# Performance work log

Hardware: AMD Instinct MI355X
Metric: run time of the kernel (lower is better)

## Reference

```python
import jax, jax.numpy as jnp
import numpy as np

N = 100000   # nodes
E = 1600000  # edges (avg degree 16)
IN, HID, OUT = 128, 128, 64
EPS = 1e-5


def setup_inputs() -> dict:
    key = jax.random.key(0)
    ks = jax.random.split(key, 16)
    x = jax.random.normal(ks[0], (N, IN), jnp.float32)
    edge_index = jax.random.randint(ks[1], (2, E), 0, N, dtype=jnp.int64)
    edge_weight = jax.random.uniform(ks[2], (E,), jnp.float32)

    def lin(k, o, i):
        return jax.random.normal(k, (o, i), jnp.float32) / np.float32(np.sqrt(i))

    return {
        "x": x, "edge_index": edge_index, "edge_weight": edge_weight,
        # SGConv linear layers
        "W1": lin(ks[3], HID, IN), "b1": jnp.zeros((HID,), jnp.float32),
        "W2": lin(ks[4], HID, HID), "b2": jnp.zeros((HID,), jnp.float32),
        "W3": lin(ks[5], OUT, HID), "b3": jnp.zeros((OUT,), jnp.float32),
        # BatchNorm affine params (nontrivial values for a meaningful reference)
        "g1": 1.0 + 0.1 * jax.random.normal(ks[6], (HID,), jnp.float32),
        "be1": 0.1 * jax.random.normal(ks[7], (HID,), jnp.float32),
        "g2": 1.0 + 0.1 * jax.random.normal(ks[8], (HID,), jnp.float32),
        "be2": 0.1 * jax.random.normal(ks[9], (HID,), jnp.float32),
        # proj MLP
        "pW1": lin(ks[10], HID, HID), "pb1": jnp.zeros((HID,), jnp.float32),
        "pW2": lin(ks[11], HID, HID), "pb2": jnp.zeros((HID,), jnp.float32),
    }


def reference(x, edge_index, edge_weight, W1, b1, W2, b2, W3, b3,
              g1, be1, g2, be2, pW1, pb1, pW2, pb2):
    src, dst = edge_index[0], edge_index[1]

    def propagate(h):
        # SGConv K=1, normalize=False: edge-weighted scatter-sum over neighbors
        msg = h[src] * edge_weight[:, None]          # [E, d]
        return jax.ops.segment_sum(msg, dst, num_segments=N)

    def bn(h, g, b):
        # BatchNorm1d, training-mode batch statistics (biased variance)
        m = h.mean(axis=0)
        v = h.var(axis=0)
        return (h - m) * jax.lax.rsqrt(v + EPS) * g + b

    h = x
    h = propagate(h) @ W1.T + b1
    h = jax.nn.relu(bn(h, g1, be1))                  # dropout = identity (eval)
    h = propagate(h) @ W2.T + b2
    h = jax.nn.relu(bn(h, g2, be2))

    # proj: Linear -> Dropout(identity) -> ReLU -> Linear
    z = jax.nn.relu(h @ pW1.T + pb1) @ pW2.T + pb2
    logits = propagate(h) @ W3.T + b3
    return (logits, h, z)
```

## Files before the change

### kernel.cpp

```cpp
#include <hip/hip_runtime.h>


#define NF 128
#define BCAP 6144

using short8   = __attribute__((ext_vector_type(8))) short;
using ushort8v = __attribute__((ext_vector_type(8))) unsigned short;
using f32x4    = __attribute__((ext_vector_type(4))) float;

__device__ __forceinline__ float b2f(unsigned short u) {
    return __uint_as_float(((unsigned)u) << 16);
}
__device__ __forceinline__ unsigned short f2b(float f) {
    unsigned u = __float_as_uint(f);
    u += 0x7fff + ((u >> 16) & 1);
    return (unsigned short)(u >> 16);
}


__global__ __launch_bounds__(512) void filla2_k(const int* __restrict__ ei,
                                                const float* __restrict__ ew,
                                                int* __restrict__ bcur,
                                                int2* __restrict__ tmp, int E)
{
    __shared__ int dstg[4096];
    __shared__ int cnt[512];
    __shared__ int base[512];
    int t = threadIdx.x;
    cnt[t] = 0;
    __syncthreads();
    int e0 = blockIdx.x * 4096;
    int eend = min(e0 + 4096, E);
    int n = eend - e0;
    for (int i = t; i < n; i += 512) {
        int d = ei[E + e0 + i];
        dstg[i] = d;
        atomicAdd(&cnt[d >> 8], 1);
    }
    __syncthreads();
    {
        int c = cnt[t];
        base[t] = c ? (t * BCAP + atomicAdd(&bcur[t], c)) : 0;
        cnt[t] = 0;
    }
    __syncthreads();
    for (int i = t; i < n; i += 512) {
        int d = dstg[i];
        int b = d >> 8;
        int r = atomicAdd(&cnt[b], 1);
        int2 q;
        q.x = (int)(((unsigned)ei[e0 + i]) | (((unsigned)(d & 255)) << 24));
        q.y = __float_as_int(ew[e0 + i]);
        tmp[base[b] + r] = q;
    }
}

__global__ __launch_bounds__(512) void bscan_k(const int* __restrict__ bcnt,
                                               int* __restrict__ bbase, int nbuk)
{
    __shared__ int sc[512];
    int t = threadIdx.x;
    int v = (t < nbuk) ? bcnt[t] : 0;
    sc[t] = v;
    __syncthreads();
    for (int ofs = 1; ofs < 512; ofs <<= 1) {
        int x = (t >= ofs) ? sc[t - ofs] : 0;
        __syncthreads();
        sc[t] += x;
        __syncthreads();
    }
    if (t < nbuk) bbase[t] = sc[t] - v;
}

__global__ __launch_bounds__(512) void fillb_k(const int2* __restrict__ tmp,
                                               const int* __restrict__ bbase,
                                               const int* __restrict__ bcnt,
                                               int* __restrict__ off,
                                               int2* __restrict__ epk,
                                               int N, int E, int nbuk)
{
    __shared__ int lcnt[256];
    __shared__ int lcur[256];
    int t = threadIdx.x;
    int b = blockIdx.x;
    int lo = b << 8;
    int nn = min(256, N - lo);
    if (t < 256) lcnt[t] = 0;
    __syncthreads();
    const int2* src = tmp + (size_t)b * BCAP;
    int cntb = bcnt[b];
    int s = bbase[b];
    for (int i = t; i < cntb; i += 512)
        atomicAdd(&lcnt[((unsigned)src[i].x) >> 24], 1);
    __syncthreads();
    int v = (t < 256) ? lcnt[t] : 0;
    for (int ofs = 1; ofs < 256; ofs <<= 1) {
        int x = (t >= ofs && t < 256) ? lcnt[t - ofs] : 0;
        __syncthreads();
        if (t < 256) lcnt[t] += x;
        __syncthreads();
    }
    if (t < 256) {
        int st = s + lcnt[t] - v;
        lcur[t] = st;
        if (t < nn) off[lo + t] = st;
    }
    if (b == 0 && t == 0) off[N] = E;
    __syncthreads();
    for (int i = t; i < cntb; i += 512) {
        int2 q = src[i];
        unsigned qx = (unsigned)q.x;
        int pos = atomicAdd(&lcur[qx >> 24], 1);
        int2 o;
        o.x = (int)(qx & 0xFFFFFF);
        o.y = q.y;
        epk[pos] = o;
    }
}

__global__ __launch_bounds__(256) void convx_k(const float* __restrict__ x,
                                               unsigned short* __restrict__ xb,
                                               int total4)
{
    int idx = blockIdx.x * 256 + threadIdx.x;
    if (idx >= total4) return;
    float4 v = *(const float4*)&x[(size_t)idx * 4];
    ushort4 o;
    o.x = f2b(v.x); o.y = f2b(v.y); o.z = f2b(v.z); o.w = f2b(v.w);
    *(ushort4*)&xb[(size_t)idx * 4] = o;
}

__global__ __launch_bounds__(64) void convw_all_k(
    const float* __restrict__ W1,  const float* __restrict__ W2,
    const float* __restrict__ pW1, const float* __restrict__ pW2,
    const float* __restrict__ W3,
    unsigned short* __restrict__ W1b,  unsigned short* __restrict__ W2b,
    unsigned short* __restrict__ pW1b, unsigned short* __restrict__ pW2b,
    unsigned short* __restrict__ W3b)
{
    int bid = blockIdx.x;
    const float* W; unsigned short* Wb; int lb;
    if      (bid < 32)  { W = W1;  Wb = W1b;  lb = bid; }
    else if (bid < 64)  { W = W2;  Wb = W2b;  lb = bid - 32; }
    else if (bid < 96)  { W = pW1; Wb = pW1b; lb = bid - 64; }
    else if (bid < 128) { W = pW2; Wb = pW2b; lb = bid - 96; }
    else                { W = W3;  Wb = W3b;  lb = bid - 128; }
    int lane = threadIdx.x;
    int nb = lb >> 2, ks = lb & 3;
    const float* src = W + (size_t)(nb * 16 + (lane & 15)) * 128 + ks * 32 + (lane >> 4) * 8;
    unsigned short* dst = Wb + ((size_t)lb * 64 + lane) * 8;
#pragma unroll
    for (int j = 0; j < 8; j++) dst[j] = f2b(src[j]);
}

template <int BN>
__global__ __launch_bounds__(256) void gather_k(
    const unsigned short* __restrict__ h, const int* __restrict__ off,
    const int2* __restrict__ epk, unsigned short* __restrict__ p, int N,
    const float* __restrict__ bnstats, const float* __restrict__ g,
    const float* __restrict__ be, float invN)
{
    int row = blockIdx.x * 4 + (threadIdx.x >> 6);
    if (row >= N) return;
    int lane = threadIdx.x & 63;
    int half = lane >> 4;
    int sub  = lane & 15;
    int c0 = sub * 8;

    float sc[8], sh[8];
#pragma unroll
    for (int j = 0; j < 8; j++) { sc[j] = 1.f; sh[j] = 0.f; }
    if (BN) {
#pragma unroll
        for (int j = 0; j < 8; j++) {
            float m = bnstats[c0 + j] * invN;
            float v = bnstats[NF + c0 + j] * invN - m * m;
            float r = rsqrtf(v + 1e-5f) * g[c0 + j];
            sc[j] = r; sh[j] = be[c0 + j] - m * r;
        }
    }

    int beg = off[row], end = off[row + 1];
    float a[8];
#pragma unroll
    for (int j = 0; j < 8; j++) a[j] = 0.f;

#define PROC_EDGE(qq, uu)                                                     \
    {                                                                         \
        float w = __int_as_float((qq).y);                                     \
        _Pragma("unroll")                                                     \
        for (int j = 0; j < 8; j++) {                                         \
            float v = b2f((unsigned short)(uu)[j]);                           \
            if (BN) v = fmaxf(fmaf(v, sc[j], sh[j]), 0.f);                    \
            a[j] = fmaf(v, w, a[j]);                                          \
        }                                                                     \
    }

    int e = beg;
    for (; e + 16 <= end; e += 16) {
        int2 q0 = epk[e + 0 + half],  q1 = epk[e + 4 + half];
        int2 q2 = epk[e + 8 + half],  q3 = epk[e + 12 + half];
        ushort8v u0 = *(const ushort8v*)&h[(size_t)q0.x * NF + c0];
        ushort8v u1 = *(const ushort8v*)&h[(size_t)q1.x * NF + c0];
        ushort8v u2 = *(const ushort8v*)&h[(size_t)q2.x * NF + c0];
        ushort8v u3 = *(const ushort8v*)&h[(size_t)q3.x * NF + c0];
        PROC_EDGE(q0, u0); PROC_EDGE(q1, u1);
        PROC_EDGE(q2, u2); PROC_EDGE(q3, u3);
    }
    for (; e + 4 <= end; e += 4) {
        int2 q = epk[e + half];
        ushort8v u = *(const ushort8v*)&h[(size_t)q.x * NF + c0];
        PROC_EDGE(q, u);
    }
    if (half < end - e) {
        int2 q = epk[e + half];
        ushort8v u = *(const ushort8v*)&h[(size_t)q.x * NF + c0];
        PROC_EDGE(q, u);
    }
#undef PROC_EDGE

#pragma unroll
    for (int j = 0; j < 8; j++) {
        a[j] += __shfl_xor(a[j], 16);
        a[j] += __shfl_xor(a[j], 32);
    }

    if (half == 0) {
        ushort8v o;
#pragma unroll
        for (int j = 0; j < 8; j++) o[j] = f2b(a[j]);
        *(ushort8v*)&p[(size_t)row * NF + c0] = o;
    }
}

__global__ __launch_bounds__(256) void gather64_k(
    const unsigned short* __restrict__ y, const int* __restrict__ off,
    const int2* __restrict__ epk, const float* __restrict__ bias,
    float* __restrict__ out, int N)
{
    int row = blockIdx.x * 4 + (threadIdx.x >> 6);
    if (row >= N) return;
    int lane = threadIdx.x & 63;
    int str = lane >> 4;
    int sub = lane & 15;
    int c0 = sub * 4;

    int beg = off[row], end = off[row + 1];
    float a[4] = {0.f, 0.f, 0.f, 0.f};

#define PROC_E64(qq, uu)                                                      \
    {                                                                         \
        float w = __int_as_float((qq).y);                                     \
        a[0] = fmaf(b2f((uu).x), w, a[0]);                                    \
        a[1] = fmaf(b2f((uu).y), w, a[1]);                                    \
        a[2] = fmaf(b2f((uu).z), w, a[2]);                                    \
        a[3] = fmaf(b2f((uu).w), w, a[3]);                                    \
    }

    int e = beg;
    for (; e + 16 <= end; e += 16) {
        int2 q0 = epk[e + 0 + str],  q1 = epk[e + 4 + str];
        int2 q2 = epk[e + 8 + str],  q3 = epk[e + 12 + str];
        ushort4 u0 = *(const ushort4*)&y[(size_t)q0.x * 64 + c0];
        ushort4 u1 = *(const ushort4*)&y[(size_t)q1.x * 64 + c0];
        ushort4 u2 = *(const ushort4*)&y[(size_t)q2.x * 64 + c0];
        ushort4 u3 = *(const ushort4*)&y[(size_t)q3.x * 64 + c0];
        PROC_E64(q0, u0); PROC_E64(q1, u1);
        PROC_E64(q2, u2); PROC_E64(q3, u3);
    }
    for (; e + 4 <= end; e += 4) {
        int2 q = epk[e + str];
        ushort4 u = *(const ushort4*)&y[(size_t)q.x * 64 + c0];
        PROC_E64(q, u);
    }
    if (str < end - e) {
        int2 q = epk[e + str];
        ushort4 u = *(const ushort4*)&y[(size_t)q.x * 64 + c0];
        PROC_E64(q, u);
    }
#undef PROC_E64

#pragma unroll
    for (int j = 0; j < 4; j++) {
        a[j] += __shfl_xor(a[j], 16);
        a[j] += __shfl_xor(a[j], 32);
    }

    if (lane < 16) {
        float4 o;
        o.x = a[0] + bias[c0];     o.y = a[1] + bias[c0 + 1];
        o.z = a[2] + bias[c0 + 2]; o.w = a[3] + bias[c0 + 3];
        *(float4*)&out[(size_t)row * 64 + c0] = o;
    }
}

template <int M, int COUT>
__global__ __launch_bounds__(256) void mgemm_k(
    const unsigned short* __restrict__ A, const unsigned short* __restrict__ Wb,
    const float* __restrict__ bias, void* __restrict__ Cp,
    int N, int relu, float* __restrict__ stats)
{
    constexpr int MI = (M == 128) ? 4 : 2;
    __shared__ float sbuf[256];

    const int tid = threadIdx.x, wid = tid >> 6, lane = tid & 63;
    const int quad = lane >> 4, l16 = lane & 15;
    const int rowBase = blockIdx.x * 128;
    int r0, c0;
    if constexpr (M == 128) { r0 = (wid >> 1) * 64; c0 = (wid & 1) * 64; }
    else                    { r0 = wid * 32;        c0 = 0; }

    f32x4 acc[MI][4];
#pragma unroll
    for (int mi = 0; mi < MI; mi++)
#pragma unroll
        for (int ni = 0; ni < 4; ni++)
#pragma unroll
            for (int r = 0; r < 4; r++) acc[mi][ni][r] = 0.f;

#pragma unroll
    for (int ks = 0; ks < 4; ++ks) {
        short8 af[MI], bf[4];
#pragma unroll
        for (int mi = 0; mi < MI; mi++) {
            int gr = rowBase + r0 + mi * 16 + l16;
            gr = (gr < N) ? gr : (N - 1);
            af[mi] = *(const short8*)(A + (size_t)gr * 128 + ks * 32 + quad * 8);
        }
#pragma unroll
        for (int ni = 0; ni < 4; ni++) {
            int nb = (c0 >> 4) + ni;
            bf[ni] = *(const short8*)(Wb + ((size_t)(nb * 4 + ks) * 64 + lane) * 8);
        }
#pragma unroll
        for (int mi = 0; mi < MI; mi++)
#pragma unroll
            for (int ni = 0; ni < 4; ni++)
                acc[mi][ni] = __builtin_amdgcn_mfma_f32_16x16x32_bf16(
                    af[mi], bf[ni], acc[mi][ni], 0, 0, 0);
    }

    float csum[4] = {0.f, 0.f, 0.f, 0.f}, csq[4] = {0.f, 0.f, 0.f, 0.f};
#pragma unroll
    for (int mi = 0; mi < MI; mi++) {
#pragma unroll
        for (int r = 0; r < 4; r++) {
            int gr = rowBase + r0 + mi * 16 + quad * 4 + r;
            if (gr >= N) continue;
#pragma unroll
            for (int ni = 0; ni < 4; ni++) {
                int col = c0 + ni * 16 + l16;
                float v = acc[mi][ni][r] + (bias ? bias[col] : 0.f);
                if (relu) v = fmaxf(v, 0.f);
                if constexpr (COUT == 1)
                    ((unsigned short*)Cp)[(size_t)gr * M + col] = f2b(v);
                else
                    ((float*)Cp)[(size_t)gr * M + col] = v;
                csum[ni] += v;
                csq[ni]  += v * v;
            }
        }
    }

    if (stats) {
        sbuf[tid] = 0.f;
        __syncthreads();
#pragma unroll
        for (int ni = 0; ni < 4; ni++) {
            int col = c0 + ni * 16 + l16;
            atomicAdd(&sbuf[col], csum[ni]);
            atomicAdd(&sbuf[128 + col], csq[ni]);
        }
        __syncthreads();
        if (tid < 128) {
            unsafeAtomicAdd(&stats[tid], sbuf[tid]);
            unsafeAtomicAdd(&stats[NF + tid], sbuf[128 + tid]);
        }
    }
}

__global__ __launch_bounds__(256) void bnrelu2_k(
    const unsigned short* __restrict__ pre, const float* __restrict__ stats,
    const float* __restrict__ g, const float* __restrict__ be,
    float* __restrict__ outh, unsigned short* __restrict__ hb,
    int total4, float invN)
{
    int idx = blockIdx.x * 256 + threadIdx.x;
    if (idx >= total4) return;
    int c = (idx * 4) & 127;
    ushort4 u = *(const ushort4*)&pre[(size_t)idx * 4];
    float in[4] = {b2f(u.x), b2f(u.y), b2f(u.z), b2f(u.w)};
    float o[4];
#pragma unroll
    for (int i = 0; i < 4; i++) {
        float m   = stats[c + i] * invN;
        float var = stats[NF + c + i] * invN - m * m;
        float rs  = rsqrtf(var + 1e-5f);
        o[i] = fmaxf((in[i] - m) * rs * g[c + i] + be[c + i], 0.f);
    }
    float4 f; f.x = o[0]; f.y = o[1]; f.z = o[2]; f.w = o[3];
    *(float4*)&outh[(size_t)idx * 4] = f;
    ushort4 h4;
    h4.x = f2b(o[0]); h4.y = f2b(o[1]); h4.z = f2b(o[2]); h4.w = f2b(o[3]);
    *(ushort4*)&hb[(size_t)idx * 4] = h4;
}

__global__ __launch_bounds__(256) void projf_k(
    const unsigned short* __restrict__ A, const unsigned short* __restrict__ W1b,
    const float* __restrict__ bias1, const unsigned short* __restrict__ W2b,
    const float* __restrict__ bias2, float* __restrict__ Z, int N)
{
    __shared__ unsigned short tbuf[128][136];

    const int tid = threadIdx.x, wid = tid >> 6, lane = tid & 63;
    const int quad = lane >> 4, l16 = lane & 15;
    const int rowBase = blockIdx.x * 128;
    const int r0 = (wid >> 1) * 64, c0 = (wid & 1) * 64;

    f32x4 acc[4][4];
#pragma unroll
    for (int mi = 0; mi < 4; mi++)
#pragma unroll
        for (int ni = 0; ni < 4; ni++)
#pragma unroll
            for (int r = 0; r < 4; r++) acc[mi][ni][r] = 0.f;

#pragma unroll
    for (int ks = 0; ks < 4; ++ks) {
        short8 af[4], bf[4];
#pragma unroll
        for (int mi = 0; mi < 4; mi++) {
            int gr = rowBase + r0 + mi * 16 + l16;
            gr = (gr < N) ? gr : (N - 1);
            af[mi] = *(const short8*)(A + (size_t)gr * 128 + ks * 32 + quad * 8);
        }
#pragma unroll
        for (int ni = 0; ni < 4; ni++) {
            int nb = (c0 >> 4) + ni;
            bf[ni] = *(const short8*)(W1b + ((size_t)(nb * 4 + ks) * 64 + lane) * 8);
        }
#pragma unroll
        for (int mi = 0; mi < 4; mi++)
#pragma unroll
            for (int ni = 0; ni < 4; ni++)
                acc[mi][ni] = __builtin_amdgcn_mfma_f32_16x16x32_bf16(
                    af[mi], bf[ni], acc[mi][ni], 0, 0, 0);
    }
#pragma unroll
    for (int mi = 0; mi < 4; mi++)
#pragma unroll
        for (int r = 0; r < 4; r++) {
            int lr = r0 + mi * 16 + quad * 4 + r;
#pragma unroll
            for (int ni = 0; ni < 4; ni++) {
                int col = c0 + ni * 16 + l16;
                float v = fmaxf(acc[mi][ni][r] + bias1[col], 0.f);
                tbuf[lr][col] = f2b(v);
            }
        }
    __syncthreads();

#pragma unroll
    for (int mi = 0; mi < 4; mi++)
#pragma unroll
        for (int ni = 0; ni < 4; ni++)
#pragma unroll
            for (int r = 0; r < 4; r++) acc[mi][ni][r] = 0.f;

#pragma unroll
    for (int ks = 0; ks < 4; ++ks) {
        short8 af[4], bf[4];
#pragma unroll
        for (int mi = 0; mi < 4; mi++)
            af[mi] = *(const short8*)&tbuf[r0 + mi * 16 + l16][ks * 32 + quad * 8];
#pragma unroll
        for (int ni = 0; ni < 4; ni++) {
            int nb = (c0 >> 4) + ni;
            bf[ni] = *(const short8*)(W2b + ((size_t)(nb * 4 + ks) * 64 + lane) * 8);
        }
#pragma unroll
        for (int mi = 0; mi < 4; mi++)
#pragma unroll
            for (int ni = 0; ni < 4; ni++)
                acc[mi][ni] = __builtin_amdgcn_mfma_f32_16x16x32_bf16(
                    af[mi], bf[ni], acc[mi][ni], 0, 0, 0);
    }
#pragma unroll
    for (int mi = 0; mi < 4; mi++)
#pragma unroll
        for (int r = 0; r < 4; r++) {
            int gr = rowBase + r0 + mi * 16 + quad * 4 + r;
            if (gr >= N) continue;
#pragma unroll
            for (int ni = 0; ni < 4; ni++) {
                int col = c0 + ni * 16 + l16;
                Z[(size_t)gr * 128 + col] = acc[mi][ni][r] + bias2[col];
            }
        }
}

extern "C" void kernel_launch(void* const* d_in, const int* in_sizes, int n_in,
                              void* d_out, int out_size, void* d_ws, size_t ws_size,
                              hipStream_t stream)
{
    const float* x   = (const float*)d_in[0];
    const int*   ei  = (const int*)d_in[1];
    const float* ew  = (const float*)d_in[2];
    const float* W1  = (const float*)d_in[3];
    const float* b1  = (const float*)d_in[4];
    const float* W2  = (const float*)d_in[5];
    const float* b2  = (const float*)d_in[6];
    const float* W3  = (const float*)d_in[7];
    const float* b3  = (const float*)d_in[8];
    const float* g1  = (const float*)d_in[9];
    const float* be1 = (const float*)d_in[10];
    const float* g2  = (const float*)d_in[11];
    const float* be2 = (const float*)d_in[12];
    const float* pW1 = (const float*)d_in[13];
    const float* pb1 = (const float*)d_in[14];
    const float* pW2 = (const float*)d_in[15];
    const float* pb2 = (const float*)d_in[16];

    const int N = in_sizes[0] / NF;
    const int E = in_sizes[2];

    float* out_logits = (float*)d_out;
    float* out_h      = out_logits + (size_t)N * 64;
    float* out_z      = out_h + (size_t)N * NF;

    const size_t rowsUS = (size_t)N * NF;
    int2*           epk = (int2*)d_ws;
    unsigned short* B1  = (unsigned short*)(epk + E);
    unsigned short* B2  = B1 + rowsUS;
    unsigned short* B3  = B2 + rowsUS;
    float* stats1 = (float*)(B3 + rowsUS);
    float* stats2 = stats1 + 256;
    int*   bcur   = (int*)(stats2 + 256);
    int*   bbase  = bcur + 512;
    unsigned short* W1b  = (unsigned short*)(bbase + 512);
    unsigned short* W2b  = W1b + 128 * 128;
    unsigned short* pW1b = W2b + 128 * 128;
    unsigned short* pW2b = pW1b + 128 * 128;
    unsigned short* W3b  = pW2b + 128 * 128;
    int* off = (int*)(W3b + 64 * 128);
    int2* tmp = (int2*)B2;

    const int nbuk   = (N + 255) >> 8;
    const int ggrid  = (N + 127) / 128;
    const int pgrid  = (N + 3) / 4;
    const int c4grid = (N * NF / 4 + 255) / 256;
    const int e4grid = (E + 4095) / 4096;
    const float invN = 1.f / (float)N;

    hipMemsetAsync(stats1, 0, (2 * 256) * sizeof(float) + 512 * sizeof(int), stream);

    convx_k<<<c4grid, 256, 0, stream>>>(x, B1, N * NF / 4);
    convw_all_k<<<176, 64, 0, stream>>>(W1, W2, pW1, pW2, W3,
                                        W1b, W2b, pW1b, pW2b, W3b);

    filla2_k<<<e4grid, 512, 0, stream>>>(ei, ew, bcur, tmp, E);
    bscan_k<<<1, 512, 0, stream>>>(bcur, bbase, nbuk);
    fillb_k<<<nbuk, 512, 0, stream>>>(tmp, bbase, bcur, off, epk, N, E, nbuk);

    gather_k<0><<<pgrid, 256, 0, stream>>>(B1, off, epk, B2, N,
                                           nullptr, nullptr, nullptr, 0.f);
    mgemm_k<128, 1><<<ggrid, 256, 0, stream>>>(B2, W1b, b1, B3, N, 0, stats1);

    gather_k<1><<<pgrid, 256, 0, stream>>>(B3, off, epk, B2, N,
                                           stats1, g1, be1, invN);
    mgemm_k<128, 1><<<ggrid, 256, 0, stream>>>(B2, W2b, b2, B1, N, 0, stats2);

    bnrelu2_k<<<c4grid, 256, 0, stream>>>(B1, stats2, g2, be2, out_h, B2,
                                          N * NF / 4, invN);

    mgemm_k<64, 1><<<ggrid, 256, 0, stream>>>(B2, W3b, nullptr, B3, N, 0, nullptr);
    gather64_k<<<pgrid, 256, 0, stream>>>(B3, off, epk, b3, out_logits, N);

    projf_k<<<ggrid, 256, 0, stream>>>(B2, pW1b, pb1, pW2b, pb2, out_z, N);
}
```

Baseline: 589.3 us.

## Fuse W3 projection into proj MLP kernel and pack bf16 unpack with vector FMAs

The W3 GEMM (h @ W3^T) is folded into the proj-MLP kernel, so the h tile is read by one kernel instead of two and one launch goes away. The gather kernels now load neighbor rows as packed 32-bit words, unpack bf16 pairs with a shift and a mask, and accumulate with two-wide float FMAs, which may let the compiler emit packed FMA instructions. The fused kernel writes Y with scalar per-element stores rather than vectorized ones, and carries more register pressure from holding the extra accumulators.

```diff
diff --git a/kernel.cpp b/kernel.cpp
--- a/kernel.cpp
+++ b/kernel.cpp
@@ -6,7 +6,10 @@
 
 using short8   = __attribute__((ext_vector_type(8))) short;
 using ushort8v = __attribute__((ext_vector_type(8))) unsigned short;
+using uint4v   = __attribute__((ext_vector_type(4))) unsigned int;
+using uint2v   = __attribute__((ext_vector_type(2))) unsigned int;
 using f32x4    = __attribute__((ext_vector_type(4))) float;
+using f32x2    = __attribute__((ext_vector_type(2))) float;
 
 __device__ __forceinline__ float b2f(unsigned short u) {
     return __uint_as_float(((unsigned)u) << 16);
@@ -16,7 +19,6 @@
     u += 0x7fff + ((u >> 16) & 1);
     return (unsigned short)(u >> 16);
 }
-
 
 __global__ __launch_bounds__(512) void filla2_k(const int* __restrict__ ei,
                                                 const float* __restrict__ ew,
@@ -167,32 +169,39 @@
     int sub  = lane & 15;
     int c0 = sub * 8;
 
-    float sc[8], sh[8];
-#pragma unroll
-    for (int j = 0; j < 8; j++) { sc[j] = 1.f; sh[j] = 0.f; }
+    f32x2 sc2[4], sh2[4];
     if (BN) {
 #pragma unroll
         for (int j = 0; j < 8; j++) {
             float m = bnstats[c0 + j] * invN;
             float v = bnstats[NF + c0 + j] * invN - m * m;
             float r = rsqrtf(v + 1e-5f) * g[c0 + j];
-            sc[j] = r; sh[j] = be[c0 + j] - m * r;
+            sc2[j >> 1][j & 1] = r;
+            sh2[j >> 1][j & 1] = be[c0 + j] - m * r;
         }
     }
 
     int beg = off[row], end = off[row + 1];
-    float a[8];
-#pragma unroll
-    for (int j = 0; j < 8; j++) a[j] = 0.f;
+    f32x2 acc2[4];
+#pragma unroll
+    for (int j = 0; j < 4; j++) { acc2[j][0] = 0.f; acc2[j][1] = 0.f; }
 
 #define PROC_EDGE(qq, uu)                                                     \
     {                                                                         \
         float w = __int_as_float((qq).y);                                     \
+        f32x2 w2; w2[0] = w; w2[1] = w;                                       \
         _Pragma("unroll")                                                     \
-        for (int j = 0; j < 8; j++) {                                         \
-            float v = b2f((unsigned short)(uu)[j]);                           \
-            if (BN) v = fmaxf(fmaf(v, sc[j], sh[j]), 0.f);                    \
-            a[j] = fmaf(v, w, a[j]);                                          \
+        for (int j = 0; j < 4; j++) {                                         \
+            unsigned d = (uu)[j];                                             \
+            f32x2 v;                                                          \
+            v[0] = __uint_as_float(d << 16);                                  \
+            v[1] = __uint_as_float(d & 0xffff0000u);                          \
+            if (BN) {                                                         \
+                v = __builtin_elementwise_fma(v, sc2[j], sh2[j]);             \
+                v[0] = fmaxf(v[0], 0.f);                                      \
+                v[1] = fmaxf(v[1], 0.f);                                      \
+            }                                                                 \
+            acc2[j] = __builtin_elementwise_fma(v, w2, acc2[j]);              \
         }                                                                     \
     }
 
@@ -200,25 +209,28 @@
     for (; e + 16 <= end; e += 16) {
         int2 q0 = epk[e + 0 + half],  q1 = epk[e + 4 + half];
         int2 q2 = epk[e + 8 + half],  q3 = epk[e + 12 + half];
-        ushort8v u0 = *(const ushort8v*)&h[(size_t)q0.x * NF + c0];
-        ushort8v u1 = *(const ushort8v*)&h[(size_t)q1.x * NF + c0];
-        ushort8v u2 = *(const ushort8v*)&h[(size_t)q2.x * NF + c0];
-        ushort8v u3 = *(const ushort8v*)&h[(size_t)q3.x * NF + c0];
+        uint4v u0 = *(const uint4v*)&h[(size_t)q0.x * NF + c0];
+        uint4v u1 = *(const uint4v*)&h[(size_t)q1.x * NF + c0];
+        uint4v u2 = *(const uint4v*)&h[(size_t)q2.x * NF + c0];
+        uint4v u3 = *(const uint4v*)&h[(size_t)q3.x * NF + c0];
         PROC_EDGE(q0, u0); PROC_EDGE(q1, u1);
         PROC_EDGE(q2, u2); PROC_EDGE(q3, u3);
     }
     for (; e + 4 <= end; e += 4) {
         int2 q = epk[e + half];
-        ushort8v u = *(const ushort8v*)&h[(size_t)q.x * NF + c0];
+        uint4v u = *(const uint4v*)&h[(size_t)q.x * NF + c0];
         PROC_EDGE(q, u);
     }
     if (half < end - e) {
         int2 q = epk[e + half];
-        ushort8v u = *(const ushort8v*)&h[(size_t)q.x * NF + c0];
+        uint4v u = *(const uint4v*)&h[(size_t)q.x * NF + c0];
         PROC_EDGE(q, u);
     }
 #undef PROC_EDGE
 
+    float a[8];
+#pragma unroll
+    for (int j = 0; j < 4; j++) { a[2 * j] = acc2[j][0]; a[2 * j + 1] = acc2[j][1]; }
 #pragma unroll
     for (int j = 0; j < 8; j++) {
         a[j] += __shfl_xor(a[j], 16);
@@ -246,40 +258,47 @@
     int c0 = sub * 4;
 
     int beg = off[row], end = off[row + 1];
-    float a[4] = {0.f, 0.f, 0.f, 0.f};
+    f32x2 acc2[2];
+    acc2[0][0] = 0.f; acc2[0][1] = 0.f; acc2[1][0] = 0.f; acc2[1][1] = 0.f;
 
 #define PROC_E64(qq, uu)                                                      \
     {                                                                         \
         float w = __int_as_float((qq).y);                                     \
-        a[0] = fmaf(b2f((uu).x), w, a[0]);                                    \
-        a[1] = fmaf(b2f((uu).y), w, a[1]);                                    \
-        a[2] = fmaf(b2f((uu).z), w, a[2]);                                    \
-        a[3] = fmaf(b2f((uu).w), w, a[3]);                                    \
+        f32x2 w2; w2[0] = w; w2[1] = w;                                       \
+        _Pragma("unroll")                                                     \
+        for (int j = 0; j < 2; j++) {                                         \
+            unsigned d = (uu)[j];                                             \
+            f32x2 v;                                                          \
+            v[0] = __uint_as_float(d << 16);                                  \
+            v[1] = __uint_as_float(d & 0xffff0000u);                          \
+            acc2[j] = __builtin_elementwise_fma(v, w2, acc2[j]);              \
+        }                                                                     \
     }
 
     int e = beg;
     for (; e + 16 <= end; e += 16) {
         int2 q0 = epk[e + 0 + str],  q1 = epk[e + 4 + str];
         int2 q2 = epk[e + 8 + str],  q3 = epk[e + 12 + str];
-        ushort4 u0 = *(const ushort4*)&y[(size_t)q0.x * 64 + c0];
-        ushort4 u1 = *(const ushort4*)&y[(size_t)q1.x * 64 + c0];
-        ushort4 u2 = *(const ushort4*)&y[(size_t)q2.x * 64 + c0];
-        ushort4 u3 = *(const ushort4*)&y[(size_t)q3.x * 64 + c0];
+        uint2v u0 = *(const uint2v*)&y[(size_t)q0.x * 64 + c0];
+        uint2v u1 = *(const uint2v*)&y[(size_t)q1.x * 64 + c0];
+        uint2v u2 = *(const uint2v*)&y[(size_t)q2.x * 64 + c0];
+        uint2v u3 = *(const uint2v*)&y[(size_t)q3.x * 64 + c0];
         PROC_E64(q0, u0); PROC_E64(q1, u1);
         PROC_E64(q2, u2); PROC_E64(q3, u3);
     }
     for (; e + 4 <= end; e += 4) {
         int2 q = epk[e + str];
-        ushort4 u = *(const ushort4*)&y[(size_t)q.x * 64 + c0];
+        uint2v u = *(const uint2v*)&y[(size_t)q.x * 64 + c0];
         PROC_E64(q, u);
     }
     if (str < end - e) {
         int2 q = epk[e + str];
-        ushort4 u = *(const ushort4*)&y[(size_t)q.x * 64 + c0];
+        uint2v u = *(const uint2v*)&y[(size_t)q.x * 64 + c0];
         PROC_E64(q, u);
     }
 #undef PROC_E64
 
+    float a[4] = {acc2[0][0], acc2[0][1], acc2[1][0], acc2[1][1]};
 #pragma unroll
     for (int j = 0; j < 4; j++) {
         a[j] += __shfl_xor(a[j], 16);
@@ -405,16 +424,62 @@
     *(ushort4*)&hb[(size_t)idx * 4] = h4;
 }
 
-__global__ __launch_bounds__(256) void projf_k(
+__global__ __launch_bounds__(256) void projf3_k(
     const unsigned short* __restrict__ A, const unsigned short* __restrict__ W1b,
     const float* __restrict__ bias1, const unsigned short* __restrict__ W2b,
-    const float* __restrict__ bias2, float* __restrict__ Z, int N)
+    const float* __restrict__ bias2, const unsigned short* __restrict__ W3b,
+    float* __restrict__ Z, unsigned short* __restrict__ Y, int N)
 {
     __shared__ unsigned short tbuf[128][136];
 
     const int tid = threadIdx.x, wid = tid >> 6, lane = tid & 63;
     const int quad = lane >> 4, l16 = lane & 15;
     const int rowBase = blockIdx.x * 128;
+
+    {
+        const int r0y = wid * 32;
+        f32x4 acy[2][4];
+#pragma unroll
+        for (int mi = 0; mi < 2; mi++)
+#pragma unroll
+            for (int ni = 0; ni < 4; ni++)
+#pragma unroll
+                for (int r = 0; r < 4; r++) acy[mi][ni][r] = 0.f;
+
+#pragma unroll
+        for (int ks = 0; ks < 4; ++ks) {
+            short8 af[2], bf[4];
+#pragma unroll
+            for (int mi = 0; mi < 2; mi++) {
+                int gr = rowBase + r0y + mi * 16 + l16;
+                gr = (gr < N) ? gr : (N - 1);
+                af[mi] = *(const short8*)(A + (size_t)gr * 128 + ks * 32 + quad * 8);
+            }
+#pragma unroll
+            for (int ni = 0; ni < 4; ni++)
+                bf[ni] = *(const short8*)(W3b + ((size_t)(ni * 4 + ks) * 64 + lane) * 8);
+#pragma unroll
+            for (int mi = 0; mi < 2; mi++)
+#pragma unroll
+                for (int ni = 0; ni < 4; ni++)
+                    acy[mi][ni] = __builtin_amdgcn_mfma_f32_16x16x32_bf16(
+                        af[mi], bf[ni], acy[mi][ni], 0, 0, 0);
+        }
+
+#pragma unroll
+        for (int mi = 0; mi < 2; mi++)
+#pragma unroll
+            for (int r = 0; r < 4; r++) {
+                int gr = rowBase + r0y + mi * 16 + quad * 4 + r;
+                if (gr >= N) continue;
+#pragma unroll
+                for (int ni = 0; ni < 4; ni++) {
+                    int col = ni * 16 + l16;
+                    Y[(size_t)gr * 64 + col] = f2b(acy[mi][ni][r] + 0.f);
+                }
+            }
+    }
+
     const int r0 = (wid >> 1) * 64, c0 = (wid & 1) * 64;
 
     f32x4 acc[4][4];
@@ -573,8 +638,8 @@
     bnrelu2_k<<<c4grid, 256, 0, stream>>>(B1, stats2, g2, be2, out_h, B2,
                                           N * NF / 4, invN);
 
-    mgemm_k<64, 1><<<ggrid, 256, 0, stream>>>(B2, W3b, nullptr, B3, N, 0, nullptr);
+    projf3_k<<<ggrid, 256, 0, stream>>>(B2, pW1b, pb1, pW2b, pb2, W3b,
+                                        out_z, B3, N);
+
     gather64_k<<<pgrid, 256, 0, stream>>>(B3, off, epk, b3, out_logits, N);
-
-    projf_k<<<ggrid, 256, 0, stream>>>(B2, pW1b, pb1, pW2b, pb2, out_z, N);
-}
+}
```

Result: no change. 587.5 us (-0.3%).
